# Kernel optimization log

Measured on AMD Instinct MI355X. Metric: run time of the kernel, lower is better.

## Reference

```python
import jax, jax.numpy as jnp
import numpy as np

N_NODES = 100000
N_FEAT = 128
HID = 8
HEADS1 = 8
OUT2 = 32
NEG_SLOPE = 0.2


def gat_conv(x, W, a_src, a_dst, b, src, dst, n_nodes, concat):
    # x: [N, Fin], W: [Fin, H*C], a_src/a_dst: [H, C], b: [H*C] or [C]
    H, C = a_src.shape
    h = (x @ W).reshape(n_nodes, H, C)                      # [N, H, C]
    e_src = jnp.sum(h * a_src, axis=-1)                     # [N, H]
    e_dst = jnp.sum(h * a_dst, axis=-1)                     # [N, H]
    e = jax.nn.leaky_relu(e_src[src] + e_dst[dst], NEG_SLOPE)  # [E, H]
    m = jax.ops.segment_max(e, dst, num_segments=n_nodes)   # [N, H] (self-loops => no empty segment)
    ex = jnp.exp(e - m[dst])                                # [E, H]
    denom = jax.ops.segment_sum(ex, dst, num_segments=n_nodes)
    alpha = ex / denom[dst]                                 # [E, H]
    out = jax.ops.segment_sum(alpha[:, :, None] * h[src], dst, num_segments=n_nodes)  # [N, H, C]
    out = out.reshape(n_nodes, H * C) if concat else out.mean(axis=1)
    return out + b


def setup_inputs() -> dict:
    key = jax.random.key(0)
    ks = jax.random.split(key, 12)
    x = jax.random.normal(ks[0], (N_NODES, N_FEAT), dtype=jnp.float32)
    edge_index = jax.random.randint(ks[1], (2, 3200000), 0, N_NODES, dtype=jnp.int64)
    s1 = 1.0 / np.sqrt(N_FEAT)
    s2 = 1.0 / np.sqrt(HID * HEADS1)
    return {
        "x": x,
        "edge_index": edge_index,
        "W1": jax.random.normal(ks[2], (N_FEAT, HEADS1 * HID), dtype=jnp.float32) * s1,
        "a_src1": jax.random.normal(ks[3], (HEADS1, HID), dtype=jnp.float32) * s2,
        "a_dst1": jax.random.normal(ks[4], (HEADS1, HID), dtype=jnp.float32) * s2,
        "b1": jnp.zeros((HEADS1 * HID,), dtype=jnp.float32),
        "W2": jax.random.normal(ks[5], (HEADS1 * HID, OUT2), dtype=jnp.float32) * s2,
        "a_src2": jax.random.normal(ks[6], (1, OUT2), dtype=jnp.float32) * (1.0 / np.sqrt(OUT2)),
        "a_dst2": jax.random.normal(ks[7], (1, OUT2), dtype=jnp.float32) * (1.0 / np.sqrt(OUT2)),
        "b2": jnp.zeros((OUT2,), dtype=jnp.float32),
        "Wr": jax.random.normal(ks[8], (OUT2, 1), dtype=jnp.float32) * (1.0 / np.sqrt(OUT2)),
        "br": jnp.zeros((1,), dtype=jnp.float32),
    }


def reference(x, edge_index, W1, a_src1, a_dst1, b1, W2, a_src2, a_dst2, b2, Wr, br):
    n = x.shape[0]
    # PyG GATConv default add_self_loops=True
    loops = jnp.arange(n, dtype=edge_index.dtype)
    src = jnp.concatenate([edge_index[0], loops])
    dst = jnp.concatenate([edge_index[1], loops])
    h = gat_conv(x, W1, a_src1, a_dst1, b1, src, dst, n, concat=True)   # [N, 64]
    h = jax.nn.elu(h)
    h = gat_conv(h, W2, a_src2, a_dst2, b2, src, dst, n, concat=False)  # [N, 32]
    pooled = jnp.sum(h, axis=0, keepdims=True)                          # SumAggregation -> [1, 32]
    return pooled @ Wr + br                                             # [1, 1]
```

## Files before the change

### kernel.cpp

```cpp
#include <hip/hip_runtime.h>
#include <math.h>

#define NEG_SLOPE 0.2f
#define FIN 128
#define H1 8
#define F1 64
#define F2 32

#define SHIFT 5
#define BW 32
#define CAPL 2048
#define CAP_G 1408
#define NBMAX 4096

#define SB_SHIFT 11
#define NSBMAX 64
#define P_CHUNK 2048
#define BPS 35
#define SBCAP (BPS * P_CHUNK)

typedef unsigned short ushort_t;
typedef unsigned int uint_t;

#define LO16(u) __uint_as_float((u) << 16)
#define HI16(u) __uint_as_float((u) & 0xffff0000u)

static __device__ __forceinline__ ushort_t f2bf(float f) {
    uint_t u = __float_as_uint(f);
    u = (u + 0x7FFFu + ((u >> 16) & 1u)) >> 16;
    return (ushort_t)u;
}
static __device__ __forceinline__ float bf2f(ushort_t h) {
    return __uint_as_float(((uint_t)h) << 16);
}
static __device__ __forceinline__ uint_t packAB(float e) {
    return (uint_t)f2bf(__expf(e)) | ((uint_t)f2bf(__expf(NEG_SLOPE * e)) << 16);
}

__global__ void gemm1_kernel(const float* __restrict__ x, const float* __restrict__ W1,
                             const float* __restrict__ a_src, const float* __restrict__ a_dst,
                             ushort_t* __restrict__ h1, uint_t* __restrict__ sp,
                             float* __restrict__ ed, int N) {
    __shared__ float xs[16][FIN];
    int tid = threadIdx.x;
    int n0 = blockIdx.x * 16;
    for (int i = tid; i < 16 * FIN; i += 256) {
        int nn = n0 + (i >> 7);
        xs[i >> 7][i & 127] = (nn < N) ? x[(size_t)nn * FIN + (i & 127)] : 0.f;
    }
    __syncthreads();
    int wv = tid >> 6, j = tid & 63;
    int nb = wv << 2;
    float a0 = 0.f, a1 = 0.f, a2 = 0.f, a3 = 0.f;
#pragma unroll 2
    for (int k = 0; k < FIN; k += 4) {
        float w0 = W1[(k + 0) * F1 + j];
        float w1 = W1[(k + 1) * F1 + j];
        float w2 = W1[(k + 2) * F1 + j];
        float w3 = W1[(k + 3) * F1 + j];
        float4 x0 = *(const float4*)&xs[nb + 0][k];
        float4 x1 = *(const float4*)&xs[nb + 1][k];
        float4 x2 = *(const float4*)&xs[nb + 2][k];
        float4 x3 = *(const float4*)&xs[nb + 3][k];
        a0 = fmaf(x0.x, w0, fmaf(x0.y, w1, fmaf(x0.z, w2, fmaf(x0.w, w3, a0))));
        a1 = fmaf(x1.x, w0, fmaf(x1.y, w1, fmaf(x1.z, w2, fmaf(x1.w, w3, a1))));
        a2 = fmaf(x2.x, w0, fmaf(x2.y, w1, fmaf(x2.z, w2, fmaf(x2.w, w3, a2))));
        a3 = fmaf(x3.x, w0, fmaf(x3.y, w1, fmaf(x3.z, w2, fmaf(x3.w, w3, a3))));
    }
    float as = a_src[j], ad = a_dst[j];
    float av[4] = {a0, a1, a2, a3};
#pragma unroll
    for (int t = 0; t < 4; ++t) {
        int n = n0 + nb + t;
        if (n >= N) break;
        h1[(size_t)n * F1 + j] = f2bf(av[t]);
        float vs = av[t] * as;
        float vd = av[t] * ad;
#pragma unroll
        for (int off = 4; off >= 1; off >>= 1) {
            vs += __shfl_down(vs, off, 8);
            vd += __shfl_down(vd, off, 8);
        }
        if ((j & 7) == 0) {
            sp[n * H1 + (j >> 3)] = packAB(vs);
            ed[n * H1 + (j >> 3)] = vd;
        }
    }
}

__global__ void zerob_kernel(int* __restrict__ bcnt, int* __restrict__ boff,
                             int NB, float* __restrict__ pooled, int capg,
                             int* __restrict__ sbcnt, int nsb) {
    int t = blockIdx.x * blockDim.x + threadIdx.x;
    int stride = gridDim.x * blockDim.x;
    for (int i = t; i < NB; i += stride) {
        bcnt[i] = 0;
        if (capg) boff[i] = i * capg;
    }
    for (int i = t; i < nsb; i += stride) sbcnt[i] = 0;
    if (t == 0) pooled[0] = 0.f;
}

__global__ void __launch_bounds__(256, 4)
part1_kernel(const int* __restrict__ ei, int E, int N,
             int* __restrict__ sbcnt, uint_t* __restrict__ sbdata) {
    __shared__ int hist[NSBMAX];
    __shared__ int loff[NSBMAX];
    __shared__ int lcur[NSBMAX];
    __shared__ int gb[NSBMAX];
    __shared__ uint_t buf[P_CHUNK];
    __shared__ unsigned char sbarr[P_CHUNK];
    int tid = threadIdx.x;
    int NSB = (N + ((1 << SB_SHIFT) - 1)) >> SB_SHIFT;
    for (int i = tid; i < NSB; i += 256) hist[i] = 0;
    __syncthreads();
    int EN = E + N;
    int base = blockIdx.x * P_CHUNK;
    int m = EN - base; if (m > P_CHUNK) m = P_CHUNK;
    int t0 = base + tid * 8;
    int s[8], d[8];
    bool fast = (t0 + 8 <= E) && ((E & 3) == 0);
    if (fast) {
        int4 a = *(const int4*)&ei[t0];
        int4 b = *(const int4*)&ei[t0 + 4];
        s[0]=a.x; s[1]=a.y; s[2]=a.z; s[3]=a.w; s[4]=b.x; s[5]=b.y; s[6]=b.z; s[7]=b.w;
        int4 c = *(const int4*)&ei[E + t0];
        int4 e2 = *(const int4*)&ei[E + t0 + 4];
        d[0]=c.x; d[1]=c.y; d[2]=c.z; d[3]=c.w; d[4]=e2.x; d[5]=e2.y; d[6]=e2.z; d[7]=e2.w;
    } else {
#pragma unroll
        for (int r = 0; r < 8; ++r) {
            int t = t0 + r;
            if (t < EN) {
                if (t < E) { s[r] = ei[t]; d[r] = ei[E + t]; }
                else       { s[r] = d[r] = t - E; }
            } else d[r] = -1;
        }
    }
#pragma unroll
    for (int r = 0; r < 8; ++r)
        if (d[r] >= 0) atomicAdd(&hist[d[r] >> SB_SHIFT], 1);
    __syncthreads();
    if (tid < 64) {
        int v = (tid < NSB) ? hist[tid] : 0;
        int e = v;
#pragma unroll
        for (int o = 1; o < 64; o <<= 1) {
            int u = __shfl_up(e, o, 64);
            if (tid >= o) e += u;
        }
        e -= v;
        if (tid < NSB) {
            loff[tid] = e;
            lcur[tid] = e;
            gb[tid] = v ? atomicAdd(&sbcnt[tid], v) : 0;
        }
    }
    __syncthreads();
#pragma unroll
    for (int r = 0; r < 8; ++r)
        if (d[r] >= 0) {
            int sb = d[r] >> SB_SHIFT;
            int pos = atomicAdd(&lcur[sb], 1);
            buf[pos] = ((uint_t)s[r] << SB_SHIFT) | (uint_t)(d[r] & ((1 << SB_SHIFT) - 1));
            sbarr[pos] = (unsigned char)sb;
        }
    __syncthreads();
    for (int i = tid; i < m; i += 256) {
        int sb = sbarr[i];
        int idx = gb[sb] + (i - loff[sb]);
        if (idx < SBCAP)
            sbdata[(size_t)sb * SBCAP + idx] = buf[i];
    }
}

__global__ void __launch_bounds__(256, 4)
part2_kernel(const uint_t* __restrict__ sbdata, const int* __restrict__ sbcnt,
             int* __restrict__ bcnt, const int* __restrict__ boff,
             uint_t* __restrict__ pk) {
    __shared__ int hist[64];
    __shared__ int loff[64];
    __shared__ int lcur[64];
    __shared__ int gb[64];
    __shared__ uint_t buf[P_CHUNK];
    int tid = threadIdx.x;
    int sb = blockIdx.x / BPS;
    int base = (blockIdx.x % BPS) * P_CHUNK;
    int cnt = sbcnt[sb];
    if (cnt > SBCAP) cnt = SBCAP;
    if (base >= cnt) return;
    int m = cnt - base; if (m > P_CHUNK) m = P_CHUNK;
    if (tid < 64) hist[tid] = 0;
    __syncthreads();
    const uint_t* src = sbdata + (size_t)sb * SBCAP + base;
    uint_t v[8];
#pragma unroll
    for (int r = 0; r < 8; ++r) {
        int i = tid + r * 256;
        if (i < m) {
            v[r] = src[i];
            atomicAdd(&hist[(v[r] >> 5) & 63], 1);
        }
    }
    __syncthreads();
    if (tid < 64) {
        int c = hist[tid];
        int e = c;
#pragma unroll
        for (int o = 1; o < 64; o <<= 1) {
            int u = __shfl_up(e, o, 64);
            if (tid >= o) e += u;
        }
        e -= c;
        loff[tid] = e;
        lcur[tid] = e;
        int bucket = (sb << 6) + tid;
        gb[tid] = c ? (boff[bucket] + atomicAdd(&bcnt[bucket], c)) : 0;
    }
    __syncthreads();
#pragma unroll
    for (int r = 0; r < 8; ++r) {
        int i = tid + r * 256;
        if (i < m) {
            int lb = (v[r] >> 5) & 63;
            int pos = atomicAdd(&lcur[lb], 1);
            buf[pos] = v[r];
        }
    }
    __syncthreads();
    for (int i = tid; i < m; i += 256) {
        uint_t u = buf[i];
        int lb = (u >> 5) & 63;
        int idx = gb[lb] + (i - loff[lb]);
        pk[idx] = ((u >> SB_SHIFT) << SHIFT) | (u & (BW - 1));
    }
}

__global__ void bhist_kernel(const int* __restrict__ ei, int E, int N,
                             int* __restrict__ bcnt, int NB) {
    __shared__ int h[NBMAX];
    int tid = threadIdx.x;
    for (int i = tid; i < NB; i += 256) h[i] = 0;
    __syncthreads();
    int EN = E + N;
    int chunk = (EN + gridDim.x - 1) / gridDim.x;
    int e0 = blockIdx.x * chunk;
    int e1 = e0 + chunk; if (e1 > EN) e1 = EN;
    for (int t = e0 + tid; t < e1; t += 256) {
        int d = (t < E) ? ei[E + t] : (t - E);
        atomicAdd(&h[d >> SHIFT], 1);
    }
    __syncthreads();
    for (int i = tid; i < NB; i += 256)
        if (h[i]) atomicAdd(&bcnt[i], h[i]);
}

__global__ void bscan_kernel(const int* __restrict__ bcnt, int NB,
                             int* __restrict__ boff, int* __restrict__ bcur) {
    int lane = threadIdx.x;
    int chunk = (NB + 63) >> 6;
    int lo = lane * chunk;
    int hi = lo + chunk; if (hi > NB) hi = NB;
    int sum = 0;
    for (int i = lo; i < hi; ++i) sum += bcnt[i];
    int e = sum;
#pragma unroll
    for (int o = 1; o < 64; o <<= 1) {
        int v = __shfl_up(e, o, 64);
        if (lane >= o) e += v;
    }
    e -= sum;
    int run = e;
    for (int i = lo; i < hi; ++i) {
        int c = bcnt[i];
        boff[i] = run;
        bcur[i] = run;
        run += c;
    }
}

__global__ void bscat_kernel(const int* __restrict__ ei, int E, int N,
                             int* __restrict__ bcur, uint_t* __restrict__ pk, int NB) {
    __shared__ int lh[NBMAX];
    __shared__ int lc[NBMAX];
    int tid = threadIdx.x;
    for (int i = tid; i < NB; i += 256) lh[i] = 0;
    __syncthreads();
    int EN = E + N;
    int chunk = (EN + gridDim.x - 1) / gridDim.x;
    int e0 = blockIdx.x * chunk;
    int e1 = e0 + chunk; if (e1 > EN) e1 = EN;
    for (int t = e0 + tid; t < e1; t += 256) {
        int d = (t < E) ? ei[E + t] : (t - E);
        atomicAdd(&lh[d >> SHIFT], 1);
    }
    __syncthreads();
    for (int i = tid; i < NB; i += 256) {
        int c = lh[i];
        lc[i] = c ? atomicAdd(&bcur[i], c) : 0;
    }
    __syncthreads();
    for (int t = e0 + tid; t < e1; t += 256) {
        int s, d;
        if (t < E) { s = ei[t]; d = ei[E + t]; } else { s = d = t - E; }
        int pos = atomicAdd(&lc[d >> SHIFT], 1);
        pk[pos] = ((uint_t)s << SHIFT) | (uint_t)(d & (BW - 1));
    }
}

__global__ void __launch_bounds__(256, 8)
edge1_gather(const int* __restrict__ bcnt, const int* __restrict__ boff,
             const uint_t* __restrict__ pk,
             const uint_t* __restrict__ sp, const float* __restrict__ ed,
             const ushort_t* __restrict__ h1, float* __restrict__ o1, int N) {
    int b = blockIdx.x;
    int d0 = b << SHIFT;
    int cnt = bcnt[b];
    int gbase = boff[b];
    int tid = threadIdx.x;
    int wv = tid >> 6;
    int L = tid & 63;
    int q = L >> 4;
    int c4 = (L & 15) << 2;
    int hL = (L & 15) >> 1;
    __shared__ int ldeg[BW];
    __shared__ int loff[BW];
    __shared__ int lcur[BW];
    __shared__ int lsrc[CAPL];
    if (cnt <= CAPL) {
        if (tid < BW) ldeg[tid] = 0;
        __syncthreads();
        for (int k = tid; k < cnt; k += 256) atomicAdd(&ldeg[pk[gbase + k] & (BW - 1)], 1);
        __syncthreads();
        if (tid < BW) {
            int v = ldeg[tid];
            int e = v;
#pragma unroll
            for (int o = 1; o < BW; o <<= 1) {
                int u = __shfl_up(e, o, 64);
                if (tid >= o) e += u;
            }
            e -= v;
            loff[tid] = e;
            lcur[tid] = e;
        }
        __syncthreads();
        for (int k = tid; k < cnt; k += 256) {
            uint_t v = pk[gbase + k];
            int pos = atomicAdd(&lcur[v & (BW - 1)], 1);
            lsrc[pos] = (int)(v >> SHIFT);
        }
        __syncthreads();
        for (int ld = wv * 8; ld < wv * 8 + 8; ++ld) {
            int d = d0 + ld;
            if (d >= N) break;
            int st = loff[ld], en = st + ldeg[ld];
            float edv = ed[d * H1 + hL];
            float Ad = __expf(edv), Bd = __expf(NEG_SLOPE * edv);
            float ax = 0.f, ay = 0.f, az = 0.f, aw = 0.f, wsum = 0.f;
            uint_t U0, U1; uint2 V0, V1;
            {
                int i0 = st + q, i1 = st + 4 + q;
                bool ok0 = i0 < en, ok1 = i1 < en;
                int s0 = lsrc[ok0 ? i0 : st];
                int s1 = lsrc[ok1 ? i1 : st];
                uint_t u0 = sp[s0 * H1 + hL];
                uint_t u1 = sp[s1 * H1 + hL];
                V0 = *(const uint2*)(h1 + ((size_t)s0 << 6) + c4);
                V1 = *(const uint2*)(h1 + ((size_t)s1 << 6) + c4);
                U0 = ok0 ? u0 : 0u;
                U1 = ok1 ? u1 : 0u;
            }
            for (int k = st; k < en; k += 8) {
                uint_t N0, N1; uint2 P0, P1;
                {
                    int i0 = k + 8 + q, i1 = k + 12 + q;
                    bool ok0 = i0 < en, ok1 = i1 < en;
                    int s0 = lsrc[ok0 ? i0 : st];
                    int s1 = lsrc[ok1 ? i1 : st];
                    uint_t u0 = sp[s0 * H1 + hL];
                    uint_t u1 = sp[s1 * H1 + hL];
                    P0 = *(const uint2*)(h1 + ((size_t)s0 << 6) + c4);
                    P1 = *(const uint2*)(h1 + ((size_t)s1 << 6) + c4);
                    N0 = ok0 ? u0 : 0u;
                    N1 = ok1 ? u1 : 0u;
                }
                float w0 = fmaxf(LO16(U0) * Ad, HI16(U0) * Bd);
                float w1 = fmaxf(LO16(U1) * Ad, HI16(U1) * Bd);
                ax = fmaf(w0, LO16(V0.x), ax);
                ay = fmaf(w0, HI16(V0.x), ay);
                az = fmaf(w0, LO16(V0.y), az);
                aw = fmaf(w0, HI16(V0.y), aw);
                ax = fmaf(w1, LO16(V1.x), ax);
                ay = fmaf(w1, HI16(V1.x), ay);
                az = fmaf(w1, LO16(V1.y), az);
                aw = fmaf(w1, HI16(V1.y), aw);
                wsum += w0 + w1;
                U0 = N0; U1 = N1; V0 = P0; V1 = P1;
            }
            ax += __shfl_xor(ax, 16, 64); ax += __shfl_xor(ax, 32, 64);
            ay += __shfl_xor(ay, 16, 64); ay += __shfl_xor(ay, 32, 64);
            az += __shfl_xor(az, 16, 64); az += __shfl_xor(az, 32, 64);
            aw += __shfl_xor(aw, 16, 64); aw += __shfl_xor(aw, 32, 64);
            wsum += __shfl_xor(wsum, 16, 64); wsum += __shfl_xor(wsum, 32, 64);
            if (q == 0) {
                float inv = 1.f / wsum;
                float4 r; r.x = ax * inv; r.y = ay * inv; r.z = az * inv; r.w = aw * inv;
                *(float4*)(o1 + (size_t)d * F1 + c4) = r;
            }
        }
    } else {
        for (int ld = wv * 8; ld < wv * 8 + 8; ++ld) {
            int d = d0 + ld;
            if (d >= N) break;
            float edv = ed[d * H1 + hL];
            float Ad = __expf(edv), Bd = __expf(NEG_SLOPE * edv);
            float ax = 0.f, ay = 0.f, az = 0.f, aw = 0.f, wsum = 0.f;
            for (int k0 = 0; k0 < cnt; k0 += 4) {
                int idx = k0 + q;
                bool ok = idx < cnt;
                uint_t v = pk[gbase + (ok ? idx : 0)];
                int s = (int)(v >> SHIFT);
                bool m = ok && ((int)(v & (BW - 1)) == ld);
                uint_t u = sp[(uint_t)s * H1 + hL];
                float w = m ? fmaxf(LO16(u) * Ad, HI16(u) * Bd) : 0.f;
                uint2 hv = *(const uint2*)(h1 + ((size_t)s << 6) + c4);
                ax = fmaf(w, LO16(hv.x), ax);
                ay = fmaf(w, HI16(hv.x), ay);
                az = fmaf(w, LO16(hv.y), az);
                aw = fmaf(w, HI16(hv.y), aw);
                wsum += w;
            }
            ax += __shfl_xor(ax, 16, 64); ax += __shfl_xor(ax, 32, 64);
            ay += __shfl_xor(ay, 16, 64); ay += __shfl_xor(ay, 32, 64);
            az += __shfl_xor(az, 16, 64); az += __shfl_xor(az, 32, 64);
            aw += __shfl_xor(aw, 16, 64); aw += __shfl_xor(aw, 32, 64);
            wsum += __shfl_xor(wsum, 16, 64); wsum += __shfl_xor(wsum, 32, 64);
            if (q == 0) {
                float inv = 1.f / wsum;
                float4 r; r.x = ax * inv; r.y = ay * inv; r.z = az * inv; r.w = aw * inv;
                *(float4*)(o1 + (size_t)d * F1 + c4) = r;
            }
        }
    }
}

__global__ void gemm2_kernel(const float* __restrict__ o1, const float* __restrict__ b1,
                             const float* __restrict__ W2,
                             const float* __restrict__ a_src2, const float* __restrict__ a_dst2,
                             ushort_t* __restrict__ h2, uint_t* __restrict__ sp2,
                             float* __restrict__ ed2, int N) {
    int half = threadIdx.x >> 5;
    int n = blockIdx.x * 8 + half;
    int j = threadIdx.x & 31;
    __shared__ float a1s[8][F1];
    if (n < N) {
#pragma unroll
        for (int r = 0; r < 2; ++r) {
            int k = r * 32 + j;
            float v = o1[(size_t)n * F1 + k] + b1[k];
            a1s[half][k] = v > 0.f ? v : expm1f(v);
        }
    }
    __syncthreads();
    if (n >= N) return;
    float acc = 0.f;
#pragma unroll
    for (int k = 0; k < F1; ++k) acc = fmaf(a1s[half][k], W2[k * F2 + j], acc);
    h2[(size_t)n * F2 + j] = f2bf(acc);
    float vs = acc * a_src2[j];
    float vd = acc * a_dst2[j];
#pragma unroll
    for (int off = 16; off >= 1; off >>= 1) {
        vs += __shfl_down(vs, off, 32);
        vd += __shfl_down(vd, off, 32);
    }
    if (j == 0) {
        sp2[n] = packAB(vs);
        ed2[n] = vd;
    }
}

__global__ void __launch_bounds__(256, 8)
edge2_gather(const int* __restrict__ bcnt, const int* __restrict__ boff,
             const uint_t* __restrict__ pk,
             const uint_t* __restrict__ sp2, const float* __restrict__ ed2,
             const ushort_t* __restrict__ h2,
             const float* __restrict__ b2, const float* __restrict__ Wr,
             float* __restrict__ pooled, int N) {
    int b = blockIdx.x;
    int d0 = b << SHIFT;
    int cnt = bcnt[b];
    int gbase = boff[b];
    int tid = threadIdx.x;
    int wv = tid >> 6;
    int L = tid & 63;
    int q = L >> 4;
    int cc = (L & 15) << 1;
    __shared__ int ldeg[BW];
    __shared__ int loff[BW];
    __shared__ int lcur[BW];
    __shared__ int lsrc[CAPL];
    float wr0 = Wr[cc], wr1 = Wr[cc + 1];
    float b2w = b2[cc] * wr0 + b2[cc + 1] * wr1;
    float part = 0.f;
    if (cnt <= CAPL) {
        if (tid < BW) ldeg[tid] = 0;
        __syncthreads();
        for (int k = tid; k < cnt; k += 256) atomicAdd(&ldeg[pk[gbase + k] & (BW - 1)], 1);
        __syncthreads();
        if (tid < BW) {
            int v = ldeg[tid];
            int e = v;
#pragma unroll
            for (int o = 1; o < BW; o <<= 1) {
                int u = __shfl_up(e, o, 64);
                if (tid >= o) e += u;
            }
            e -= v;
            loff[tid] = e;
            lcur[tid] = e;
        }
        __syncthreads();
        for (int k = tid; k < cnt; k += 256) {
            uint_t v = pk[gbase + k];
            int pos = atomicAdd(&lcur[v & (BW - 1)], 1);
            lsrc[pos] = (int)(v >> SHIFT);
        }
        __syncthreads();
        for (int ld = wv * 8; ld < wv * 8 + 8; ++ld) {
            int d = d0 + ld;
            if (d >= N) break;
            int st = loff[ld], en = st + ldeg[ld];
            float edv = ed2[d];
            float Ad = __expf(edv), Bd = __expf(NEG_SLOPE * edv);
            float a0 = 0.f, a1 = 0.f, wsum = 0.f;
            uint_t U0, U1, V0, V1;
            {
                int i0 = st + q, i1 = st + 4 + q;
                bool ok0 = i0 < en, ok1 = i1 < en;
                int s0 = lsrc[ok0 ? i0 : st];
                int s1 = lsrc[ok1 ? i1 : st];
                uint_t u0 = sp2[s0];
                uint_t u1 = sp2[s1];
                V0 = *(const uint_t*)(h2 + (size_t)s0 * F2 + cc);
                V1 = *(const uint_t*)(h2 + (size_t)s1 * F2 + cc);
                U0 = ok0 ? u0 : 0u;
                U1 = ok1 ? u1 : 0u;
            }
            for (int k = st; k < en; k += 8) {
                uint_t N0, N1, P0, P1;
                {
                    int i0 = k + 8 + q, i1 = k + 12 + q;
                    bool ok0 = i0 < en, ok1 = i1 < en;
                    int s0 = lsrc[ok0 ? i0 : st];
                    int s1 = lsrc[ok1 ? i1 : st];
                    uint_t u0 = sp2[s0];
                    uint_t u1 = sp2[s1];
                    P0 = *(const uint_t*)(h2 + (size_t)s0 * F2 + cc);
                    P1 = *(const uint_t*)(h2 + (size_t)s1 * F2 + cc);
                    N0 = ok0 ? u0 : 0u;
                    N1 = ok1 ? u1 : 0u;
                }
                float w0 = fmaxf(LO16(U0) * Ad, HI16(U0) * Bd);
                float w1 = fmaxf(LO16(U1) * Ad, HI16(U1) * Bd);
                a0 = fmaf(w0, LO16(V0), a0);
                a1 = fmaf(w0, HI16(V0), a1);
                a0 = fmaf(w1, LO16(V1), a0);
                a1 = fmaf(w1, HI16(V1), a1);
                wsum += w0 + w1;
                U0 = N0; U1 = N1; V0 = P0; V1 = P1;
            }
            a0 += __shfl_xor(a0, 16, 64); a0 += __shfl_xor(a0, 32, 64);
            a1 += __shfl_xor(a1, 16, 64); a1 += __shfl_xor(a1, 32, 64);
            wsum += __shfl_xor(wsum, 16, 64); wsum += __shfl_xor(wsum, 32, 64);
            if (q == 0) {
                float inv = 1.f / wsum;
                part += (a0 * wr0 + a1 * wr1) * inv + b2w;
            }
        }
    } else {
        for (int ld = wv * 8; ld < wv * 8 + 8; ++ld) {
            int d = d0 + ld;
            if (d >= N) break;
            float edv = ed2[d];
            float Ad = __expf(edv), Bd = __expf(NEG_SLOPE * edv);
            float a0 = 0.f, a1 = 0.f, wsum = 0.f;
            for (int k0 = 0; k0 < cnt; k0 += 4) {
                int idx = k0 + q;
                bool ok = idx < cnt;
                uint_t v = pk[gbase + (ok ? idx : 0)];
                int s = (int)(v >> SHIFT);
                bool m = ok && ((int)(v & (BW - 1)) == ld);
                uint_t u = m ? sp2[s] : 0u;
                uint_t hv = *(const uint_t*)(h2 + (size_t)s * F2 + cc);
                float w = fmaxf(LO16(u) * Ad, HI16(u) * Bd);
                a0 = fmaf(w, LO16(hv), a0);
                a1 = fmaf(w, HI16(hv), a1);
                wsum += w;
            }
            a0 += __shfl_xor(a0, 16, 64); a0 += __shfl_xor(a0, 32, 64);
            a1 += __shfl_xor(a1, 16, 64); a1 += __shfl_xor(a1, 32, 64);
            wsum += __shfl_xor(wsum, 16, 64); wsum += __shfl_xor(wsum, 32, 64);
            if (q == 0) {
                float inv = 1.f / wsum;
                part += (a0 * wr0 + a1 * wr1) * inv + b2w;
            }
        }
    }
#pragma unroll
    for (int o = 32; o >= 1; o >>= 1) part += __shfl_down(part, o, 64);
    __shared__ float ls[4];
    if ((tid & 63) == 0) ls[wv] = part;
    __syncthreads();
    if (tid == 0) atomicAdd(pooled, ls[0] + ls[1] + ls[2] + ls[3]);
}

__global__ void final_kernel(const float* __restrict__ pooled, const float* __restrict__ br,
                             float* __restrict__ out) {
    if (threadIdx.x == 0 && blockIdx.x == 0) out[0] = pooled[0] + br[0];
}

extern "C" void kernel_launch(void* const* d_in, const int* in_sizes, int n_in,
                              void* d_out, int out_size, void* d_ws, size_t ws_size,
                              hipStream_t stream) {
    const float* x    = (const float*)d_in[0];
    const int*   ei   = (const int*)d_in[1];
    const float* W1   = (const float*)d_in[2];
    const float* a_s1 = (const float*)d_in[3];
    const float* a_d1 = (const float*)d_in[4];
    const float* b1   = (const float*)d_in[5];
    const float* W2   = (const float*)d_in[6];
    const float* a_s2 = (const float*)d_in[7];
    const float* a_d2 = (const float*)d_in[8];
    const float* b2   = (const float*)d_in[9];
    const float* Wr   = (const float*)d_in[10];
    const float* br   = (const float*)d_in[11];
    float* out = (float*)d_out;

    int N = in_sizes[0] / FIN;
    int E = in_sizes[1] / 2;
    size_t n = (size_t)N;
    int NB = (N + BW - 1) >> SHIFT;
    int NSB = (N + ((1 << SB_SHIFT) - 1)) >> SB_SHIFT;

    char* ws = (char*)d_ws;
    float*    o1   = (float*)ws;
    uint_t*   sp1  = (uint_t*)(ws + n * 256);
    float*    ed1  = (float*)(ws + n * 288);
    ushort_t* h1   = (ushort_t*)(ws + n * 320);
    uint_t*   pk   = (uint_t*)(ws + n * 448);
    size_t pk_static = (size_t)NB * CAP_G * 4;
    size_t pk_exact  = (size_t)(E + N) * 4;
    uint_t* sbdata = (uint_t*)ws;
    bool use_static = (NSB <= NSBMAX) &&
                      ((size_t)NSB * SBCAP * 4 <= n * 256) &&
                      (ws_size >= n * 448 + pk_static + (size_t)NBMAX * 16 + NSBMAX * 4 + 256);
    char* tail = ws + n * 448 + (use_static ? pk_static : pk_exact);
    int*      bcnt  = (int*)tail;
    int*      boff  = (int*)(tail + NBMAX * 4);
    int*      bcur  = (int*)(tail + NBMAX * 8);
    int*      sbcnt = (int*)(tail + NBMAX * 12);
    float*  pooled  = (float*)(tail + NBMAX * 12 + NSBMAX * 4);
    ushort_t* h2  = h1;
    uint_t*   sp2 = sp1;
    float*    ed2 = ed1;

    zerob_kernel<<<8, 256, 0, stream>>>(bcnt, boff, NB, pooled,
                                        use_static ? CAP_G : 0, sbcnt, NSB);
    if (use_static) {
        int EN = E + N;
        int G1 = (EN + P_CHUNK - 1) / P_CHUNK;
        part1_kernel<<<G1, 256, 0, stream>>>(ei, E, N, sbcnt, sbdata);
        part2_kernel<<<NSB * BPS, 256, 0, stream>>>(sbdata, sbcnt, bcnt, boff, pk);
        gemm1_kernel<<<(N + 15) / 16, 256, 0, stream>>>(x, W1, a_s1, a_d1, h1, sp1, ed1, N);
    } else {
        gemm1_kernel<<<(N + 15) / 16, 256, 0, stream>>>(x, W1, a_s1, a_d1, h1, sp1, ed1, N);
        bhist_kernel<<<256, 256, 0, stream>>>(ei, E, N, bcnt, NB);
        bscan_kernel<<<1, 64, 0, stream>>>(bcnt, NB, boff, bcur);
        bscat_kernel<<<256, 256, 0, stream>>>(ei, E, N, bcur, pk, NB);
    }
    edge1_gather<<<NB, 256, 0, stream>>>(bcnt, boff, pk, sp1, ed1, h1, o1, N);
    gemm2_kernel<<<(N + 7) / 8, 256, 0, stream>>>(o1, b1, W2, a_s2, a_d2, h2, sp2, ed2, N);
    edge2_gather<<<NB, 256, 0, stream>>>(bcnt, boff, pk, sp2, ed2, h2, b2, Wr, pooled, N);
    final_kernel<<<1, 64, 0, stream>>>(pooled, br, out);
}
```

Baseline: 394.2 us.

## Fold readout into layer-2 projection and use persistent padded edge gathers

Layer 2's per-node 32-dim features are replaced by a scalar projection onto Wr computed in gemm2. This works because the mean, sum pooling and readout are linear, so edge2 only gathers an 8-byte record per edge instead of a 32-wide row. Both edge gather kernels become persistent grids that pull buckets from an atomic counter. They pad each destination's edge list to a multiple of 8 using a zero sentinel node, which removes bounds checks. Edge1 now maps one head per lane with 16-byte loads, and edge2 uses all 64 lanes per destination. The cost is a tighter shared-memory cap for the fast path and more workspace layout offsets.

Result: slower. 498.7 us (+26.5%).

```diff
diff --git a/kernel.cpp b/kernel.cpp
--- a/kernel.cpp
+++ b/kernel.cpp
@@ -25,13 +25,14 @@
 #define LO16(u) __uint_as_float((u) << 16)
 #define HI16(u) __uint_as_float((u) & 0xffff0000u)
 
+#define FOLDQ(x) { x += __shfl_xor(x, 8, 64); x += __shfl_xor(x, 16, 64); x += __shfl_xor(x, 32, 64); }
+#define FOLD64(x) { x += __shfl_xor(x, 1, 64); x += __shfl_xor(x, 2, 64); x += __shfl_xor(x, 4, 64); \
+                    x += __shfl_xor(x, 8, 64); x += __shfl_xor(x, 16, 64); x += __shfl_xor(x, 32, 64); }
+
 static __device__ __forceinline__ ushort_t f2bf(float f) {
     uint_t u = __float_as_uint(f);
     u = (u + 0x7FFFu + ((u >> 16) & 1u)) >> 16;
     return (ushort_t)u;
-}
-static __device__ __forceinline__ float bf2f(ushort_t h) {
-    return __uint_as_float(((uint_t)h) << 16);
 }
 static __device__ __forceinline__ uint_t packAB(float e) {
     return (uint_t)f2bf(__expf(e)) | ((uint_t)f2bf(__expf(NEG_SLOPE * e)) << 16);
@@ -90,7 +91,9 @@
 
 __global__ void zerob_kernel(int* __restrict__ bcnt, int* __restrict__ boff,
                              int NB, float* __restrict__ pooled, int capg,
-                             int* __restrict__ sbcnt, int nsb) {
+                             int* __restrict__ sbcnt, int nsb,
+                             uint_t* __restrict__ sp1, ushort_t* __restrict__ h1,
+                             int* __restrict__ ctrs, int N) {
     int t = blockIdx.x * blockDim.x + threadIdx.x;
     int stride = gridDim.x * blockDim.x;
     for (int i = t; i < NB; i += stride) {
@@ -98,7 +101,11 @@
         if (capg) boff[i] = i * capg;
     }
     for (int i = t; i < nsb; i += stride) sbcnt[i] = 0;
-    if (t == 0) pooled[0] = 0.f;
+    if (t < H1) sp1[(size_t)N * H1 + t] = 0u;
+    if (t >= 8 && t < 8 + F1) h1[(size_t)N * F1 + (t - 8)] = 0;
+    if (t == 72) pooled[0] = 0.f;
+    if (t == 73) ctrs[0] = 0;
+    if (t == 74) ctrs[1] = 0;
 }
 
 __global__ void __launch_bounds__(256, 4)
@@ -312,134 +319,120 @@
 edge1_gather(const int* __restrict__ bcnt, const int* __restrict__ boff,
              const uint_t* __restrict__ pk,
              const uint_t* __restrict__ sp, const float* __restrict__ ed,
-             const ushort_t* __restrict__ h1, float* __restrict__ o1, int N) {
-    int b = blockIdx.x;
-    int d0 = b << SHIFT;
-    int cnt = bcnt[b];
-    int gbase = boff[b];
+             const ushort_t* __restrict__ h1, float* __restrict__ o1,
+             int* __restrict__ ctr, int NB, int N) {
     int tid = threadIdx.x;
     int wv = tid >> 6;
     int L = tid & 63;
-    int q = L >> 4;
-    int c4 = (L & 15) << 2;
-    int hL = (L & 15) >> 1;
-    __shared__ int ldeg[BW];
-    __shared__ int loff[BW];
-    __shared__ int lcur[BW];
+    int q = L >> 3;
+    int head = L & 7;
+    int c8 = head << 3;
+    __shared__ int ldeg[BW], loff[BW], ldgp[BW], lcur[BW];
     __shared__ int lsrc[CAPL];
-    if (cnt <= CAPL) {
-        if (tid < BW) ldeg[tid] = 0;
+    __shared__ int sbk, stot;
+    for (;;) {
+        if (tid == 0) sbk = atomicAdd(ctr, 1);
         __syncthreads();
-        for (int k = tid; k < cnt; k += 256) atomicAdd(&ldeg[pk[gbase + k] & (BW - 1)], 1);
-        __syncthreads();
-        if (tid < BW) {
-            int v = ldeg[tid];
-            int e = v;
-#pragma unroll
-            for (int o = 1; o < BW; o <<= 1) {
-                int u = __shfl_up(e, o, 64);
-                if (tid >= o) e += u;
-            }
-            e -= v;
-            loff[tid] = e;
-            lcur[tid] = e;
-        }
-        __syncthreads();
-        for (int k = tid; k < cnt; k += 256) {
-            uint_t v = pk[gbase + k];
-            int pos = atomicAdd(&lcur[v & (BW - 1)], 1);
-            lsrc[pos] = (int)(v >> SHIFT);
-        }
-        __syncthreads();
-        for (int ld = wv * 8; ld < wv * 8 + 8; ++ld) {
-            int d = d0 + ld;
-            if (d >= N) break;
-            int st = loff[ld], en = st + ldeg[ld];
-            float edv = ed[d * H1 + hL];
-            float Ad = __expf(edv), Bd = __expf(NEG_SLOPE * edv);
-            float ax = 0.f, ay = 0.f, az = 0.f, aw = 0.f, wsum = 0.f;
-            uint_t U0, U1; uint2 V0, V1;
-            {
-                int i0 = st + q, i1 = st + 4 + q;
-                bool ok0 = i0 < en, ok1 = i1 < en;
-                int s0 = lsrc[ok0 ? i0 : st];
-                int s1 = lsrc[ok1 ? i1 : st];
-                uint_t u0 = sp[s0 * H1 + hL];
-                uint_t u1 = sp[s1 * H1 + hL];
-                V0 = *(const uint2*)(h1 + ((size_t)s0 << 6) + c4);
-                V1 = *(const uint2*)(h1 + ((size_t)s1 << 6) + c4);
-                U0 = ok0 ? u0 : 0u;
-                U1 = ok1 ? u1 : 0u;
-            }
-            for (int k = st; k < en; k += 8) {
-                uint_t N0, N1; uint2 P0, P1;
-                {
-                    int i0 = k + 8 + q, i1 = k + 12 + q;
-                    bool ok0 = i0 < en, ok1 = i1 < en;
-                    int s0 = lsrc[ok0 ? i0 : st];
-                    int s1 = lsrc[ok1 ? i1 : st];
-                    uint_t u0 = sp[s0 * H1 + hL];
-                    uint_t u1 = sp[s1 * H1 + hL];
-                    P0 = *(const uint2*)(h1 + ((size_t)s0 << 6) + c4);
-                    P1 = *(const uint2*)(h1 + ((size_t)s1 << 6) + c4);
-                    N0 = ok0 ? u0 : 0u;
-                    N1 = ok1 ? u1 : 0u;
-                }
-                float w0 = fmaxf(LO16(U0) * Ad, HI16(U0) * Bd);
-                float w1 = fmaxf(LO16(U1) * Ad, HI16(U1) * Bd);
-                ax = fmaf(w0, LO16(V0.x), ax);
-                ay = fmaf(w0, HI16(V0.x), ay);
-                az = fmaf(w0, LO16(V0.y), az);
-                aw = fmaf(w0, HI16(V0.y), aw);
-                ax = fmaf(w1, LO16(V1.x), ax);
-                ay = fmaf(w1, HI16(V1.x), ay);
-                az = fmaf(w1, LO16(V1.y), az);
-                aw = fmaf(w1, HI16(V1.y), aw);
-                wsum += w0 + w1;
-                U0 = N0; U1 = N1; V0 = P0; V1 = P1;
-            }
-            ax += __shfl_xor(ax, 16, 64); ax += __shfl_xor(ax, 32, 64);
-            ay += __shfl_xor(ay, 16, 64); ay += __shfl_xor(ay, 32, 64);
-            az += __shfl_xor(az, 16, 64); az += __shfl_xor(az, 32, 64);
-            aw += __shfl_xor(aw, 16, 64); aw += __shfl_xor(aw, 32, 64);
-            wsum += __shfl_xor(wsum, 16, 64); wsum += __shfl_xor(wsum, 32, 64);
-            if (q == 0) {
-                float inv = 1.f / wsum;
-                float4 r; r.x = ax * inv; r.y = ay * inv; r.z = az * inv; r.w = aw * inv;
-                *(float4*)(o1 + (size_t)d * F1 + c4) = r;
-            }
-        }
-    } else {
-        for (int ld = wv * 8; ld < wv * 8 + 8; ++ld) {
-            int d = d0 + ld;
-            if (d >= N) break;
-            float edv = ed[d * H1 + hL];
-            float Ad = __expf(edv), Bd = __expf(NEG_SLOPE * edv);
-            float ax = 0.f, ay = 0.f, az = 0.f, aw = 0.f, wsum = 0.f;
-            for (int k0 = 0; k0 < cnt; k0 += 4) {
-                int idx = k0 + q;
-                bool ok = idx < cnt;
-                uint_t v = pk[gbase + (ok ? idx : 0)];
-                int s = (int)(v >> SHIFT);
-                bool m = ok && ((int)(v & (BW - 1)) == ld);
-                uint_t u = sp[(uint_t)s * H1 + hL];
-                float w = m ? fmaxf(LO16(u) * Ad, HI16(u) * Bd) : 0.f;
-                uint2 hv = *(const uint2*)(h1 + ((size_t)s << 6) + c4);
-                ax = fmaf(w, LO16(hv.x), ax);
-                ay = fmaf(w, HI16(hv.x), ay);
-                az = fmaf(w, LO16(hv.y), az);
-                aw = fmaf(w, HI16(hv.y), aw);
-                wsum += w;
-            }
-            ax += __shfl_xor(ax, 16, 64); ax += __shfl_xor(ax, 32, 64);
-            ay += __shfl_xor(ay, 16, 64); ay += __shfl_xor(ay, 32, 64);
-            az += __shfl_xor(az, 16, 64); az += __shfl_xor(az, 32, 64);
-            aw += __shfl_xor(aw, 16, 64); aw += __shfl_xor(aw, 32, 64);
-            wsum += __shfl_xor(wsum, 16, 64); wsum += __shfl_xor(wsum, 32, 64);
-            if (q == 0) {
-                float inv = 1.f / wsum;
-                float4 r; r.x = ax * inv; r.y = ay * inv; r.z = az * inv; r.w = aw * inv;
-                *(float4*)(o1 + (size_t)d * F1 + c4) = r;
+        int b = sbk;
+        if (b >= NB) break;
+        int d0 = b << SHIFT;
+        int cnt = bcnt[b];
+        int gbase = boff[b];
+        if (cnt <= CAPL - 8 * BW - 8) {
+            if (tid < BW) ldeg[tid] = 0;
+            __syncthreads();
+            for (int k = tid; k < cnt; k += 256) atomicAdd(&ldeg[pk[gbase + k] & (BW - 1)], 1);
+            __syncthreads();
+            if (tid < BW) {
+                int v = ldeg[tid];
+                int vp = (v + 7) & ~7;
+                int e = vp;
+#pragma unroll
+                for (int o = 1; o < BW; o <<= 1) {
+                    int u = __shfl_up(e, o, 64);
+                    if (tid >= o) e += u;
+                }
+                e -= vp;
+                loff[tid] = e;
+                lcur[tid] = e;
+                ldgp[tid] = vp;
+                if (tid == BW - 1) stot = e + vp;
+            }
+            __syncthreads();
+            int tot = stot;
+            for (int k = tid; k < tot + 8; k += 256) lsrc[k] = N;
+            __syncthreads();
+            for (int k = tid; k < cnt; k += 256) {
+                uint_t v = pk[gbase + k];
+                int pos = atomicAdd(&lcur[v & (BW - 1)], 1);
+                lsrc[pos] = (int)(v >> SHIFT);
+            }
+            __syncthreads();
+            for (int ld = wv * 8; ld < wv * 8 + 8; ++ld) {
+                int d = d0 + ld;
+                if (d >= N) break;
+                int st = loff[ld], en = st + ldgp[ld];
+                float edv = ed[d * H1 + head];
+                float Ad = __expf(edv), Bd = __expf(NEG_SLOPE * edv);
+                float a0=0.f,a1=0.f,a2=0.f,a3=0.f,a4=0.f,a5=0.f,a6=0.f,a7=0.f,ws=0.f;
+                int s = lsrc[st + q];
+                uint_t U = sp[s * H1 + head];
+                uint4 V = *(const uint4*)(h1 + ((size_t)s << 6) + c8);
+                for (int k = st; k < en; k += 8) {
+                    int s2 = lsrc[k + 8 + q];
+                    uint_t U2 = sp[s2 * H1 + head];
+                    uint4 V2 = *(const uint4*)(h1 + ((size_t)s2 << 6) + c8);
+                    float w = fmaxf(LO16(U) * Ad, HI16(U) * Bd);
+                    a0 = fmaf(w, LO16(V.x), a0); a1 = fmaf(w, HI16(V.x), a1);
+                    a2 = fmaf(w, LO16(V.y), a2); a3 = fmaf(w, HI16(V.y), a3);
+                    a4 = fmaf(w, LO16(V.z), a4); a5 = fmaf(w, HI16(V.z), a5);
+                    a6 = fmaf(w, LO16(V.w), a6); a7 = fmaf(w, HI16(V.w), a7);
+                    ws += w;
+                    U = U2; V = V2;
+                }
+                FOLDQ(a0); FOLDQ(a1); FOLDQ(a2); FOLDQ(a3);
+                FOLDQ(a4); FOLDQ(a5); FOLDQ(a6); FOLDQ(a7); FOLDQ(ws);
+                if (q == 0) {
+                    float inv = 1.f / ws;
+                    float4 r0; r0.x = a0*inv; r0.y = a1*inv; r0.z = a2*inv; r0.w = a3*inv;
+                    float4 r1; r1.x = a4*inv; r1.y = a5*inv; r1.z = a6*inv; r1.w = a7*inv;
+                    float* dp = o1 + (size_t)d * F1 + c8;
+                    *(float4*)dp = r0;
+                    *(float4*)(dp + 4) = r1;
+                }
+            }
+        } else {
+            for (int ld = wv * 8; ld < wv * 8 + 8; ++ld) {
+                int d = d0 + ld;
+                if (d >= N) break;
+                float edv = ed[d * H1 + head];
+                float Ad = __expf(edv), Bd = __expf(NEG_SLOPE * edv);
+                float a0=0.f,a1=0.f,a2=0.f,a3=0.f,a4=0.f,a5=0.f,a6=0.f,a7=0.f,ws=0.f;
+                for (int k0 = 0; k0 < cnt; k0 += 8) {
+                    int idx = k0 + q;
+                    bool ok = idx < cnt;
+                    uint_t v = pk[gbase + (ok ? idx : 0)];
+                    int s = (int)(v >> SHIFT);
+                    bool mm = ok && ((int)(v & (BW - 1)) == ld);
+                    uint_t U = sp[s * H1 + head];
+                    uint4 V = *(const uint4*)(h1 + ((size_t)s << 6) + c8);
+                    float w = mm ? fmaxf(LO16(U) * Ad, HI16(U) * Bd) : 0.f;
+                    a0 = fmaf(w, LO16(V.x), a0); a1 = fmaf(w, HI16(V.x), a1);
+                    a2 = fmaf(w, LO16(V.y), a2); a3 = fmaf(w, HI16(V.y), a3);
+                    a4 = fmaf(w, LO16(V.z), a4); a5 = fmaf(w, HI16(V.z), a5);
+                    a6 = fmaf(w, LO16(V.w), a6); a7 = fmaf(w, HI16(V.w), a7);
+                    ws += w;
+                }
+                FOLDQ(a0); FOLDQ(a1); FOLDQ(a2); FOLDQ(a3);
+                FOLDQ(a4); FOLDQ(a5); FOLDQ(a6); FOLDQ(a7); FOLDQ(ws);
+                if (q == 0) {
+                    float inv = 1.f / ws;
+                    float4 r0; r0.x = a0*inv; r0.y = a1*inv; r0.z = a2*inv; r0.w = a3*inv;
+                    float4 r1; r1.x = a4*inv; r1.y = a5*inv; r1.z = a6*inv; r1.w = a7*inv;
+                    float* dp = o1 + (size_t)d * F1 + c8;
+                    *(float4*)dp = r0;
+                    *(float4*)(dp + 4) = r1;
+                }
             }
         }
     }
@@ -448,8 +441,12 @@
 __global__ void gemm2_kernel(const float* __restrict__ o1, const float* __restrict__ b1,
                              const float* __restrict__ W2,
                              const float* __restrict__ a_src2, const float* __restrict__ a_dst2,
-                             ushort_t* __restrict__ h2, uint_t* __restrict__ sp2,
-                             float* __restrict__ ed2, int N) {
+                             const float* __restrict__ Wr,
+                             uint2* __restrict__ rec, float* __restrict__ ed2, int N) {
+    if (blockIdx.x == 0 && threadIdx.x == 0) {
+        uint2 z; z.x = 0u; z.y = 0u;
+        rec[N] = z;
+    }
     int half = threadIdx.x >> 5;
     int n = blockIdx.x * 8 + half;
     int j = threadIdx.x & 31;
@@ -467,16 +464,18 @@
     float acc = 0.f;
 #pragma unroll
     for (int k = 0; k < F1; ++k) acc = fmaf(a1s[half][k], W2[k * F2 + j], acc);
-    h2[(size_t)n * F2 + j] = f2bf(acc);
     float vs = acc * a_src2[j];
     float vd = acc * a_dst2[j];
+    float vg = acc * Wr[j];
 #pragma unroll
     for (int off = 16; off >= 1; off >>= 1) {
         vs += __shfl_down(vs, off, 32);
         vd += __shfl_down(vd, off, 32);
+        vg += __shfl_down(vg, off, 32);
     }
     if (j == 0) {
-        sp2[n] = packAB(vs);
+        uint2 r; r.x = packAB(vs); r.y = __float_as_uint(vg);
+        rec[n] = r;
         ed2[n] = vd;
     }
 }
@@ -484,134 +483,101 @@
 __global__ void __launch_bounds__(256, 8)
 edge2_gather(const int* __restrict__ bcnt, const int* __restrict__ boff,
              const uint_t* __restrict__ pk,
-             const uint_t* __restrict__ sp2, const float* __restrict__ ed2,
-             const ushort_t* __restrict__ h2,
+             const uint2* __restrict__ rec, const float* __restrict__ ed2,
              const float* __restrict__ b2, const float* __restrict__ Wr,
-             float* __restrict__ pooled, int N) {
-    int b = blockIdx.x;
-    int d0 = b << SHIFT;
-    int cnt = bcnt[b];
-    int gbase = boff[b];
+             float* __restrict__ pooled, int* __restrict__ ctr, int NB, int N) {
     int tid = threadIdx.x;
     int wv = tid >> 6;
     int L = tid & 63;
-    int q = L >> 4;
-    int cc = (L & 15) << 1;
-    __shared__ int ldeg[BW];
-    __shared__ int loff[BW];
-    __shared__ int lcur[BW];
+    __shared__ int ldeg[BW], loff[BW], ldgp[BW], lcur[BW];
     __shared__ int lsrc[CAPL];
-    float wr0 = Wr[cc], wr1 = Wr[cc + 1];
-    float b2w = b2[cc] * wr0 + b2[cc + 1] * wr1;
+    __shared__ int sbk, stot;
+    __shared__ float ls[4];
+    float t0 = (L < F2) ? b2[L] * Wr[L] : 0.f;
+    FOLD64(t0);
+    float b2w = t0;
     float part = 0.f;
-    if (cnt <= CAPL) {
-        if (tid < BW) ldeg[tid] = 0;
+    for (;;) {
+        if (tid == 0) sbk = atomicAdd(ctr, 1);
         __syncthreads();
-        for (int k = tid; k < cnt; k += 256) atomicAdd(&ldeg[pk[gbase + k] & (BW - 1)], 1);
-        __syncthreads();
-        if (tid < BW) {
-            int v = ldeg[tid];
-            int e = v;
-#pragma unroll
-            for (int o = 1; o < BW; o <<= 1) {
-                int u = __shfl_up(e, o, 64);
-                if (tid >= o) e += u;
-            }
-            e -= v;
-            loff[tid] = e;
-            lcur[tid] = e;
-        }
-        __syncthreads();
-        for (int k = tid; k < cnt; k += 256) {
-            uint_t v = pk[gbase + k];
-            int pos = atomicAdd(&lcur[v & (BW - 1)], 1);
-            lsrc[pos] = (int)(v >> SHIFT);
-        }
-        __syncthreads();
-        for (int ld = wv * 8; ld < wv * 8 + 8; ++ld) {
-            int d = d0 + ld;
-            if (d >= N) break;
-            int st = loff[ld], en = st + ldeg[ld];
-            float edv = ed2[d];
-            float Ad = __expf(edv), Bd = __expf(NEG_SLOPE * edv);
-            float a0 = 0.f, a1 = 0.f, wsum = 0.f;
-            uint_t U0, U1, V0, V1;
-            {
-                int i0 = st + q, i1 = st + 4 + q;
-                bool ok0 = i0 < en, ok1 = i1 < en;
-                int s0 = lsrc[ok0 ? i0 : st];
-                int s1 = lsrc[ok1 ? i1 : st];
-                uint_t u0 = sp2[s0];
-                uint_t u1 = sp2[s1];
-                V0 = *(const uint_t*)(h2 + (size_t)s0 * F2 + cc);
-                V1 = *(const uint_t*)(h2 + (size_t)s1 * F2 + cc);
-                U0 = ok0 ? u0 : 0u;
-                U1 = ok1 ? u1 : 0u;
-            }
-            for (int k = st; k < en; k += 8) {
-                uint_t N0, N1, P0, P1;
-                {
-                    int i0 = k + 8 + q, i1 = k + 12 + q;
-                    bool ok0 = i0 < en, ok1 = i1 < en;
-                    int s0 = lsrc[ok0 ? i0 : st];
-                    int s1 = lsrc[ok1 ? i1 : st];
-                    uint_t u0 = sp2[s0];
-                    uint_t u1 = sp2[s1];
-                    P0 = *(const uint_t*)(h2 + (size_t)s0 * F2 + cc);
-                    P1 = *(const uint_t*)(h2 + (size_t)s1 * F2 + cc);
-                    N0 = ok0 ? u0 : 0u;
-                    N1 = ok1 ? u1 : 0u;
-                }
-                float w0 = fmaxf(LO16(U0) * Ad, HI16(U0) * Bd);
-                float w1 = fmaxf(LO16(U1) * Ad, HI16(U1) * Bd);
-                a0 = fmaf(w0, LO16(V0), a0);
-                a1 = fmaf(w0, HI16(V0), a1);
-                a0 = fmaf(w1, LO16(V1), a0);
-                a1 = fmaf(w1, HI16(V1), a1);
-                wsum += w0 + w1;
-                U0 = N0; U1 = N1; V0 = P0; V1 = P1;
-            }
-            a0 += __shfl_xor(a0, 16, 64); a0 += __shfl_xor(a0, 32, 64);
-            a1 += __shfl_xor(a1, 16, 64); a1 += __shfl_xor(a1, 32, 64);
-            wsum += __shfl_xor(wsum, 16, 64); wsum += __shfl_xor(wsum, 32, 64);
-            if (q == 0) {
-                float inv = 1.f / wsum;
-                part += (a0 * wr0 + a1 * wr1) * inv + b2w;
-            }
-        }
-    } else {
-        for (int ld = wv * 8; ld < wv * 8 + 8; ++ld) {
-            int d = d0 + ld;
-            if (d >= N) break;
-            float edv = ed2[d];
-            float Ad = __expf(edv), Bd = __expf(NEG_SLOPE * edv);
-            float a0 = 0.f, a1 = 0.f, wsum = 0.f;
-            for (int k0 = 0; k0 < cnt; k0 += 4) {
-                int idx = k0 + q;
-                bool ok = idx < cnt;
-                uint_t v = pk[gbase + (ok ? idx : 0)];
-                int s = (int)(v >> SHIFT);
-                bool m = ok && ((int)(v & (BW - 1)) == ld);
-                uint_t u = m ? sp2[s] : 0u;
-                uint_t hv = *(const uint_t*)(h2 + (size_t)s * F2 + cc);
-                float w = fmaxf(LO16(u) * Ad, HI16(u) * Bd);
-                a0 = fmaf(w, LO16(hv), a0);
-                a1 = fmaf(w, HI16(hv), a1);
-                wsum += w;
-            }
-            a0 += __shfl_xor(a0, 16, 64); a0 += __shfl_xor(a0, 32, 64);
-            a1 += __shfl_xor(a1, 16, 64); a1 += __shfl_xor(a1, 32, 64);
-            wsum += __shfl_xor(wsum, 16, 64); wsum += __shfl_xor(wsum, 32, 64);
-            if (q == 0) {
-                float inv = 1.f / wsum;
-                part += (a0 * wr0 + a1 * wr1) * inv + b2w;
-            }
-        }
-    }
-#pragma unroll
-    for (int o = 32; o >= 1; o >>= 1) part += __shfl_down(part, o, 64);
-    __shared__ float ls[4];
-    if ((tid & 63) == 0) ls[wv] = part;
+        int b = sbk;
+        if (b >= NB) break;
+        int d0 = b << SHIFT;
+        int cnt = bcnt[b];
+        int gbase = boff[b];
+        if (cnt <= CAPL - 8 * BW - 8) {
+            if (tid < BW) ldeg[tid] = 0;
+            __syncthreads();
+            for (int k = tid; k < cnt; k += 256) atomicAdd(&ldeg[pk[gbase + k] & (BW - 1)], 1);
+            __syncthreads();
+            if (tid < BW) {
+                int v = ldeg[tid];
+                int vp = (v + 7) & ~7;
+                int e = vp;
+#pragma unroll
+                for (int o = 1; o < BW; o <<= 1) {
+                    int u = __shfl_up(e, o, 64);
+                    if (tid >= o) e += u;
+                }
+                e -= vp;
+                loff[tid] = e;
+                lcur[tid] = e;
+                ldgp[tid] = vp;
+                if (tid == BW - 1) stot = e + vp;
+            }
+            __syncthreads();
+            int tot = stot;
+            for (int k = tid; k < tot + 8; k += 256) lsrc[k] = N;
+            __syncthreads();
+            for (int k = tid; k < cnt; k += 256) {
+                uint_t v = pk[gbase + k];
+                int pos = atomicAdd(&lcur[v & (BW - 1)], 1);
+                lsrc[pos] = (int)(v >> SHIFT);
+            }
+            __syncthreads();
+            for (int ld = wv * 8; ld < wv * 8 + 8; ++ld) {
+                int d = d0 + ld;
+                if (d >= N) break;
+                int st = loff[ld], en = st + ldgp[ld];
+                float edv = ed2[d];
+                float Ad = __expf(edv), Bd = __expf(NEG_SLOPE * edv);
+                float acc = 0.f, wsm = 0.f;
+                for (int k = st; k < en; k += 64) {
+                    int i = k + L;
+                    bool ok = i < en;
+                    int s = lsrc[ok ? i : st];
+                    uint2 r = rec[s];
+                    float w = ok ? fmaxf(LO16(r.x) * Ad, HI16(r.x) * Bd) : 0.f;
+                    acc = fmaf(w, __uint_as_float(r.y), acc);
+                    wsm += w;
+                }
+                FOLD64(acc); FOLD64(wsm);
+                part += acc / wsm + b2w;
+            }
+        } else {
+            for (int ld = wv * 8; ld < wv * 8 + 8; ++ld) {
+                int d = d0 + ld;
+                if (d >= N) break;
+                float edv = ed2[d];
+                float Ad = __expf(edv), Bd = __expf(NEG_SLOPE * edv);
+                float acc = 0.f, wsm = 0.f;
+                for (int k0 = 0; k0 < cnt; k0 += 64) {
+                    int i = k0 + L;
+                    bool ok = i < cnt;
+                    uint_t v = pk[gbase + (ok ? i : 0)];
+                    int s = (int)(v >> SHIFT);
+                    bool mm = ok && ((int)(v & (BW - 1)) == ld);
+                    uint2 r = rec[s];
+                    float w = mm ? fmaxf(LO16(r.x) * Ad, HI16(r.x) * Bd) : 0.f;
+                    acc = fmaf(w, __uint_as_float(r.y), acc);
+                    wsm += w;
+                }
+                FOLD64(acc); FOLD64(wsm);
+                part += acc / wsm + b2w;
+            }
+        }
+    }
+    if (L == 0) ls[wv] = part;
     __syncthreads();
     if (tid == 0) atomicAdd(pooled, ls[0] + ls[1] + ls[2] + ls[3]);
 }
@@ -647,27 +613,31 @@
     char* ws = (char*)d_ws;
     float*    o1   = (float*)ws;
     uint_t*   sp1  = (uint_t*)(ws + n * 256);
-    float*    ed1  = (float*)(ws + n * 288);
-    ushort_t* h1   = (ushort_t*)(ws + n * 320);
-    uint_t*   pk   = (uint_t*)(ws + n * 448);
+    float*    ed1  = (float*)(ws + n * 288 + 64);
+    ushort_t* h1   = (ushort_t*)(ws + n * 320 + 64);
+    uint_t*   pk   = (uint_t*)(ws + n * 448 + 256);
     size_t pk_static = (size_t)NB * CAP_G * 4;
     size_t pk_exact  = (size_t)(E + N) * 4;
     uint_t* sbdata = (uint_t*)ws;
     bool use_static = (NSB <= NSBMAX) &&
                       ((size_t)NSB * SBCAP * 4 <= n * 256) &&
-                      (ws_size >= n * 448 + pk_static + (size_t)NBMAX * 16 + NSBMAX * 4 + 256);
-    char* tail = ws + n * 448 + (use_static ? pk_static : pk_exact);
+                      (ws_size >= n * 448 + 256 + pk_static + (size_t)NBMAX * 16 +
+                                  (size_t)NSBMAX * 4 + 64);
+    char* tail = ws + n * 448 + 256 + (use_static ? pk_static : pk_exact);
     int*      bcnt  = (int*)tail;
     int*      boff  = (int*)(tail + NBMAX * 4);
     int*      bcur  = (int*)(tail + NBMAX * 8);
     int*      sbcnt = (int*)(tail + NBMAX * 12);
     float*  pooled  = (float*)(tail + NBMAX * 12 + NSBMAX * 4);
-    ushort_t* h2  = h1;
-    uint_t*   sp2 = sp1;
-    float*    ed2 = ed1;
+    int*      ctrs  = (int*)(tail + NBMAX * 12 + NSBMAX * 4 + 8);
+    uint2* rec = (uint2*)h1;
+    float* ed2 = ed1;
+
+    int egrid = NB < 2048 ? NB : 2048;
 
     zerob_kernel<<<8, 256, 0, stream>>>(bcnt, boff, NB, pooled,
-                                        use_static ? CAP_G : 0, sbcnt, NSB);
+                                        use_static ? CAP_G : 0, sbcnt, NSB,
+                                        sp1, h1, ctrs, N);
     if (use_static) {
         int EN = E + N;
         int G1 = (EN + P_CHUNK - 1) / P_CHUNK;
@@ -680,8 +650,10 @@
         bscan_kernel<<<1, 64, 0, stream>>>(bcnt, NB, boff, bcur);
         bscat_kernel<<<256, 256, 0, stream>>>(ei, E, N, bcur, pk, NB);
     }
-    edge1_gather<<<NB, 256, 0, stream>>>(bcnt, boff, pk, sp1, ed1, h1, o1, N);
-    gemm2_kernel<<<(N + 7) / 8, 256, 0, stream>>>(o1, b1, W2, a_s2, a_d2, h2, sp2, ed2, N);
-    edge2_gather<<<NB, 256, 0, stream>>>(bcnt, boff, pk, sp2, ed2, h2, b2, Wr, pooled, N);
+    edge1_gather<<<egrid, 256, 0, stream>>>(bcnt, boff, pk, sp1, ed1, h1, o1,
+                                            ctrs + 0, NB, N);
+    gemm2_kernel<<<(N + 7) / 8, 256, 0, stream>>>(o1, b1, W2, a_s2, a_d2, Wr, rec, ed2, N);
+    edge2_gather<<<egrid, 256, 0, stream>>>(bcnt, boff, pk, rec, ed2, b2, Wr, pooled,
+                                            ctrs + 1, NB, N);
     final_kernel<<<1, 64, 0, stream>>>(pooled, br, out);
 }
```
